# Kernel tuning notes

Measured on AMD Instinct MI355X. Metric: run time of the kernel, lower is better.

Reference implementation:

```python
import jax, jax.numpy as jnp
import numpy as np
from jax import lax

B, N, D = 8, 1024, 768      # batch, tokens, feature dim
H, Y = 12, 64               # heads, head dim
M = 3072                    # hopfield memories (4*D)
STEPS = 12                  # descent steps (module default)
ALPHA = 0.1                 # SGD step size (module default)
BETA = 1.0 / np.sqrt(Y)     # attention inverse temperature
EPS = 1e-5


def setup_inputs() -> dict:
    key = jax.random.key(0)
    k0, k1, k2, k3 = jax.random.split(key, 4)
    return {
        "x": jax.random.normal(k0, (B, N, D), dtype=jnp.float32),
        "ln_gamma": jnp.ones((D,), dtype=jnp.float32),
        "ln_beta": jnp.zeros((D,), dtype=jnp.float32),
        "wq": jax.random.normal(k1, (H, Y, D), dtype=jnp.float32) * 0.02,
        "wk": jax.random.normal(k2, (H, Y, D), dtype=jnp.float32) * 0.02,
        "xi": jax.random.normal(k3, (M, D), dtype=jnp.float32) * 0.02,
    }


def _layer_norm(x, gamma, beta):
    mu = jnp.mean(x, axis=-1, keepdims=True)
    var = jnp.var(x, axis=-1, keepdims=True)
    return gamma * (x - mu) * lax.rsqrt(var + EPS) + beta


def _energy(g, wq, wk, xi):
    # Attention energy: A[b,h,m,n] = sum_y K_{hy m} Q_{hy n}
    q = jnp.einsum("hyd,bnd->bhny", wq, g)
    k = jnp.einsum("hyd,bnd->bhny", wk, g)
    logits = BETA * jnp.einsum("bhmy,bhny->bhmn", k, q)  # [B,H,N(keys),N(queries)]
    e_att = -(1.0 / BETA) * jnp.sum(jax.scipy.special.logsumexp(logits, axis=2))
    # Hopfield energy: -0.5 * sum relu(xi @ g)^2
    hid = jnp.einsum("md,bnd->bnm", xi, g)
    e_hn = -0.5 * jnp.sum(jnp.square(jax.nn.relu(hid)))
    return e_att + e_hn


_energy_grad = jax.grad(_energy)


def reference(x, ln_gamma, ln_beta, wq, wk, xi):
    def step(x, _):
        g = _layer_norm(x, ln_gamma, ln_beta)  # grad taken w.r.t. g, not through LN
        grad = _energy_grad(g, wq, wk, xi)
        return x - ALPHA * grad, None

    x, _ = lax.scan(step, x, None, length=STEPS)
    return x
```

## Files before the change

kernel.cpp:

```cpp
#include <hip/hip_runtime.h>
#include <math.h>

#define B_ 8
#define N_ 1024
#define D_ 768
#define H_ 12
#define Y_ 64
#define M_ 3072
#define STEPS_ 12
#define ALPHA_ 0.1f
#define BETA_ 0.125f
#define EPS_ 1e-5f

typedef __attribute__((ext_vector_type(8))) short bf16x8;
typedef __attribute__((ext_vector_type(8))) unsigned short u16x8;
typedef __attribute__((ext_vector_type(4))) float f32x4;

__device__ inline unsigned short f2bf(float f) {
  union { float f; unsigned int u; } v; v.f = f;
  unsigned int r = (v.u + 0x7fffu + ((v.u >> 16) & 1u)) >> 16;
  return (unsigned short)r;
}

__device__ inline void async_copy16(const void* g, void* l) {
  __builtin_amdgcn_global_load_lds(
      (const __attribute__((address_space(1))) unsigned int*)g,
      (__attribute__((address_space(3))) unsigned int*)l, 16, 0, 0);
}

__device__ inline int xcd_remap(int bid, int nwg) {
  const int qd = nwg >> 3, rm = nwg & 7;
  const int xcd = bid & 7, idx = bid >> 3;
  return (xcd < rm ? xcd * (qd + 1) : rm * (qd + 1) + (xcd - rm) * qd) + idx;
}

__global__ __launch_bounds__(256) void ln_kernel(const float* __restrict__ x,
    const float* __restrict__ gamma, const float* __restrict__ beta,
    unsigned short* __restrict__ g) {
  const int row = blockIdx.x;
  const int t = threadIdx.x;
  const float* xr = x + (size_t)row * D_;
  float v0 = xr[t], v1 = xr[t + 256], v2 = xr[t + 512];
  float s = v0 + v1 + v2;
  float sq = v0 * v0 + v1 * v1 + v2 * v2;
  #pragma unroll
  for (int off = 1; off < 64; off <<= 1) {
    s += __shfl_xor(s, off);
    sq += __shfl_xor(sq, off);
  }
  __shared__ float ss[4], ssq[4];
  const int wid = t >> 6;
  if ((t & 63) == 0) { ss[wid] = s; ssq[wid] = sq; }
  __syncthreads();
  s = ss[0] + ss[1] + ss[2] + ss[3];
  sq = ssq[0] + ssq[1] + ssq[2] + ssq[3];
  const float mu = s * (1.0f / D_);
  const float var = sq * (1.0f / D_) - mu * mu;
  const float r = rsqrtf(var + EPS_);
  unsigned short* gr = g + (size_t)row * D_;
  gr[t]       = f2bf(gamma[t]       * (v0 - mu) * r + beta[t]);
  gr[t + 256] = f2bf(gamma[t + 256] * (v1 - mu) * r + beta[t + 256]);
  gr[t + 512] = f2bf(gamma[t + 512] * (v2 - mu) * r + beta[t + 512]);
}

__global__ __launch_bounds__(256) void cvt_bf16(const float* __restrict__ in,
    unsigned short* __restrict__ out, int n) {
  int i = blockIdx.x * 256 + threadIdx.x;
  if (i < n) out[i] = f2bf(in[i]);
}

__global__ __launch_bounds__(256) void transpose_cvt(const float* __restrict__ in,
    unsigned short* __restrict__ out, int R, int C, int ldo, int koff) {
  __shared__ float tile[32][33];
  const int c0 = blockIdx.x * 32, r0 = blockIdx.y * 32;
  const int tx = threadIdx.x & 31, ty = threadIdx.x >> 5;
  #pragma unroll
  for (int i = 0; i < 32; i += 8)
    tile[ty + i][tx] = in[(size_t)(r0 + ty + i) * C + c0 + tx];
  __syncthreads();
  #pragma unroll
  for (int i = 0; i < 32; i += 8)
    out[(size_t)(c0 + ty + i) * ldo + koff + r0 + tx] = f2bf(tile[tx][ty + i]);
}

__global__ __launch_bounds__(256) void transpose_head(
    const unsigned short* __restrict__ in, int ld, int coff,
    unsigned short* __restrict__ out) {
  __shared__ unsigned short tile[64][68];
  const int n0 = blockIdx.x * 64;
  const int h = blockIdx.y;
  const int b = blockIdx.z;
  const int t = threadIdx.x;
  {
    const int tok = t >> 2, c0 = (t & 3) * 16;
    const unsigned short* src = in + ((size_t)(b * N_ + n0 + tok)) * ld + coff + h * Y_ + c0;
    u16x8 v0 = *(const u16x8*)src;
    u16x8 v1 = *(const u16x8*)(src + 8);
    #pragma unroll
    for (int i = 0; i < 8; ++i) {
      tile[tok][c0 + i] = v0[i];
      tile[tok][c0 + 8 + i] = v1[i];
    }
  }
  __syncthreads();
  {
    const int y = t >> 2, tb = (t & 3) * 16;
    u16x8 o0, o1;
    #pragma unroll
    for (int i = 0; i < 8; ++i) {
      o0[i] = tile[tb + i][y];
      o1[i] = tile[tb + 8 + i][y];
    }
    unsigned short* dst = out + ((size_t)((b * H_ + h) * Y_ + y)) * N_ + n0 + tb;
    *(u16x8*)dst = o0;
    *(u16x8*)(dst + 8) = o1;
  }
}

template <bool RELU>
__global__ __launch_bounds__(256) void gemm128(
    const unsigned short* __restrict__ A, const unsigned short* __restrict__ Bm,
    unsigned short* __restrict__ C, int N, int K, int gridN) {
  __shared__ __align__(16) unsigned short As[128 * 64];
  __shared__ __align__(16) unsigned short Bs[128 * 64];
  const int t = threadIdx.x;
  const int f = xcd_remap(blockIdx.x, gridDim.x);
  const int n0 = (f % gridN) * 128;
  const int m0 = (f / gridN) * 128;
  const int w = t >> 6;
  const int l = t & 63;
  const int wr = (w >> 1) * 64;
  const int wc = (w & 1) * 64;

  f32x4 acc[4][4];
  #pragma unroll
  for (int m = 0; m < 4; ++m)
    #pragma unroll
    for (int n = 0; n < 4; ++n) {
      f32x4 z = {0.f, 0.f, 0.f, 0.f};
      acc[m][n] = z;
    }

  for (int kt = 0; kt < K; kt += 64) {
    #pragma unroll
    for (int i = 0; i < 4; ++i) {
      const int flat = i * 4096 + t * 16;
      const int row = flat >> 7;
      const int slog = ((flat >> 4) & 7) ^ (row & 7);
      async_copy16(A + (size_t)(m0 + row) * K + kt + slog * 8, (char*)As + flat);
      async_copy16(Bm + (size_t)(n0 + row) * K + kt + slog * 8, (char*)Bs + flat);
    }
    __syncthreads();
    #pragma unroll
    for (int kk = 0; kk < 2; ++kk) {
      bf16x8 a[4], b[4];
      const int lr = l & 15;
      const int sl = kk * 4 + (l >> 4);
      #pragma unroll
      for (int m = 0; m < 4; ++m) {
        const int row = wr + m * 16 + lr;
        a[m] = *(const bf16x8*)((const char*)As + row * 128 + ((sl ^ (row & 7)) << 4));
      }
      #pragma unroll
      for (int n = 0; n < 4; ++n) {
        const int row = wc + n * 16 + lr;
        b[n] = *(const bf16x8*)((const char*)Bs + row * 128 + ((sl ^ (row & 7)) << 4));
      }
      #pragma unroll
      for (int m = 0; m < 4; ++m)
        #pragma unroll
        for (int n = 0; n < 4; ++n)
          acc[m][n] = __builtin_amdgcn_mfma_f32_16x16x32_bf16(a[m], b[n], acc[m][n], 0, 0, 0);
    }
    __syncthreads();
  }

  const int cr = (l >> 4) * 4;
  const int cc = l & 15;
  #pragma unroll
  for (int m = 0; m < 4; ++m)
    #pragma unroll
    for (int n = 0; n < 4; ++n) {
      const int col = n0 + wc + n * 16 + cc;
      #pragma unroll
      for (int j = 0; j < 4; ++j) {
        const int row = m0 + wr + m * 16 + cr + j;
        float v = acc[m][n][j];
        if (RELU) v = v > 0.f ? v : 0.f;
        C[(size_t)row * N + col] = f2bf(v);
      }
    }
}

__global__ __launch_bounds__(256) void gemm_update(
    const unsigned short* __restrict__ A1,
    const unsigned short* __restrict__ A2,
    const unsigned short* __restrict__ B2,
    float* __restrict__ x,
    float alpha) {
  __shared__ __align__(16) unsigned short As[128 * 64];
  __shared__ __align__(16) unsigned short Bs[64 * 64];
  const int t = threadIdx.x;
  const int f = xcd_remap(blockIdx.x, gridDim.x);
  const int n0 = (f % 12) * 64;
  const int m0 = (f / 12) * 128;
  const int w = t >> 6;
  const int l = t & 63;
  const int wr = (w >> 1) * 64;
  const int wc = (w & 1) * 32;

  f32x4 acc[4][2];
  #pragma unroll
  for (int m = 0; m < 4; ++m)
    #pragma unroll
    for (int n = 0; n < 2; ++n) {
      f32x4 z = {0.f, 0.f, 0.f, 0.f};
      acc[m][n] = z;
    }

  for (int kt = 0; kt < 4608; kt += 64) {
    #pragma unroll
    for (int i = 0; i < 4; ++i) {
      const int flat = i * 4096 + t * 16;
      const int row = flat >> 7;
      const int slog = ((flat >> 4) & 7) ^ (row & 7);
      const unsigned short* src = (kt < 1536)
          ? A1 + (size_t)(m0 + row) * 1536 + kt + slog * 8
          : A2 + (size_t)(m0 + row) * 3072 + (kt - 1536) + slog * 8;
      async_copy16(src, (char*)As + flat);
    }
    #pragma unroll
    for (int i = 0; i < 2; ++i) {
      const int flat = i * 4096 + t * 16;
      const int row = flat >> 7;
      const int slog = ((flat >> 4) & 7) ^ (row & 7);
      async_copy16(B2 + (size_t)(n0 + row) * 4608 + kt + slog * 8, (char*)Bs + flat);
    }
    __syncthreads();
    #pragma unroll
    for (int kk = 0; kk < 2; ++kk) {
      bf16x8 a[4], b[2];
      const int lr = l & 15;
      const int sl = kk * 4 + (l >> 4);
      #pragma unroll
      for (int m = 0; m < 4; ++m) {
        const int row = wr + m * 16 + lr;
        a[m] = *(const bf16x8*)((const char*)As + row * 128 + ((sl ^ (row & 7)) << 4));
      }
      #pragma unroll
      for (int n = 0; n < 2; ++n) {
        const int row = wc + n * 16 + lr;
        b[n] = *(const bf16x8*)((const char*)Bs + row * 128 + ((sl ^ (row & 7)) << 4));
      }
      #pragma unroll
      for (int m = 0; m < 4; ++m)
        #pragma unroll
        for (int n = 0; n < 2; ++n)
          acc[m][n] = __builtin_amdgcn_mfma_f32_16x16x32_bf16(a[m], b[n], acc[m][n], 0, 0, 0);
    }
    __syncthreads();
  }

  const int cr = (l >> 4) * 4;
  const int cc = l & 15;
  #pragma unroll
  for (int m = 0; m < 4; ++m)
    #pragma unroll
    for (int n = 0; n < 2; ++n) {
      const int col = n0 + wc + n * 16 + cc;
      #pragma unroll
      for (int j = 0; j < 4; ++j) {
        const int row = m0 + wr + m * 16 + cr + j;
        float* cp = x + (size_t)row * 768 + col;
        *cp += alpha * acc[m][n][j];
      }
    }
}

__global__ __launch_bounds__(256) void attn1_mfma(
    const unsigned short* __restrict__ qk, const unsigned short* __restrict__ kT,
    unsigned short* __restrict__ AqAk, float* __restrict__ lse) {
  __shared__ __align__(16) unsigned short Ks[64 * 64];
  __shared__ __align__(16) unsigned short KTs[64 * 64];
  __shared__ __align__(16) unsigned short Ps[4 * 16 * 64];
  const int n0 = blockIdx.x * 64;
  const int h = blockIdx.y;
  const int b = blockIdx.z;
  const int t = threadIdx.x;
  const int w = t >> 6;
  const int l = t & 63;
  const int g = l >> 4;
  const int ql = l & 15;
  char* psw = (char*)(Ps + w * 1024);
  const int LD = 1536;

  bf16x8 qf[2];
  {
    const unsigned short* qrow =
        qk + ((size_t)(b * N_ + n0 + w * 16 + ql)) * LD + h * Y_;
    qf[0] = *(const bf16x8*)(qrow + g * 8);
    qf[1] = *(const bf16x8*)(qrow + 32 + g * 8);
  }
  const unsigned short* kbase = qk + (size_t)b * N_ * LD + 768 + h * Y_;
  const unsigned short* kTbase = kT + ((size_t)(b * H_ + h)) * Y_ * N_;

  f32x4 acc[4];
  #pragma unroll
  for (int yf = 0; yf < 4; ++yf) { f32x4 z = {0.f,0.f,0.f,0.f}; acc[yf] = z; }
  float mmax = -1e30f, lsum = 0.f;

  for (int mc = 0; mc < N_; mc += 64) {
    #pragma unroll
    for (int i = 0; i < 2; ++i) {
      const int flat = i * 4096 + t * 16;
      const int row = flat >> 7;
      const int slog = ((flat >> 4) & 7) ^ (row & 7);
      async_copy16(kbase + (size_t)(mc + row) * LD + slog * 8, (char*)Ks + flat);
    }
    #pragma unroll
    for (int i = 0; i < 2; ++i) {
      const int flat = i * 4096 + t * 16;
      const int row = flat >> 7;
      const int slog = ((flat >> 4) & 7) ^ (row & 7);
      async_copy16(kTbase + (size_t)row * N_ + mc + slog * 8, (char*)KTs + flat);
    }
    __syncthreads();

    f32x4 s[4];
    #pragma unroll
    for (int f = 0; f < 4; ++f) {
      f32x4 z = {0.f,0.f,0.f,0.f}; s[f] = z;
      #pragma unroll
      for (int ks = 0; ks < 2; ++ks) {
        const int key = f * 16 + ql;
        bf16x8 a = *(const bf16x8*)((const char*)Ks + key * 128 +
                                    (((ks * 4 + g) ^ (key & 7)) << 4));
        s[f] = __builtin_amdgcn_mfma_f32_16x16x32_bf16(a, qf[ks], s[f], 0, 0, 0);
      }
    }
    float sv[4][4];
    float rm = -1e30f;
    #pragma unroll
    for (int f = 0; f < 4; ++f)
      #pragma unroll
      for (int j = 0; j < 4; ++j) {
        sv[f][j] = s[f][j] * BETA_;
        rm = fmaxf(rm, sv[f][j]);
      }
    rm = fmaxf(rm, __shfl_xor(rm, 16));
    rm = fmaxf(rm, __shfl_xor(rm, 32));
    const float nm = fmaxf(mmax, rm);
    const float sc = __expf(mmax - nm);
    float rs = 0.f;
    float pv[4][4];
    #pragma unroll
    for (int f = 0; f < 4; ++f)
      #pragma unroll
      for (int j = 0; j < 4; ++j) {
        pv[f][j] = __expf(sv[f][j] - nm);
        rs += pv[f][j];
      }
    rs += __shfl_xor(rs, 16);
    rs += __shfl_xor(rs, 32);
    lsum = lsum * sc + rs;
    mmax = nm;
    #pragma unroll
    for (int yf = 0; yf < 4; ++yf) acc[yf] *= sc;
    #pragma unroll
    for (int f = 0; f < 4; ++f) {
      unsigned long long pk =
          (unsigned long long)f2bf(pv[f][0]) |
          ((unsigned long long)f2bf(pv[f][1]) << 16) |
          ((unsigned long long)f2bf(pv[f][2]) << 32) |
          ((unsigned long long)f2bf(pv[f][3]) << 48);
      const int sl = (f * 4 + g) ^ ((ql & 7) << 1);
      *(unsigned long long*)(psw + ql * 128 + sl * 8) = pk;
    }
    #pragma unroll
    for (int ks2 = 0; ks2 < 2; ++ks2) {
      const int sl2 = (ks2 * 8 + g * 2) ^ ((ql & 7) << 1);
      bf16x8 pa = *(const bf16x8*)(psw + ql * 128 + sl2 * 8);
      #pragma unroll
      for (int yf = 0; yf < 4; ++yf) {
        const int y = yf * 16 + ql;
        bf16x8 bk = *(const bf16x8*)((const char*)KTs + y * 128 +
                                     (((ks2 * 4 + g) ^ (y & 7)) << 4));
        acc[yf] = __builtin_amdgcn_mfma_f32_16x16x32_bf16(pa, bk, acc[yf], 0, 0, 0);
      }
    }
    __syncthreads();
  }

  float linv[4];
  #pragma unroll
  for (int j = 0; j < 4; ++j)
    linv[j] = 1.0f / __shfl(lsum, (g << 4) + g * 4 + j);
  #pragma unroll
  for (int yf = 0; yf < 4; ++yf)
    #pragma unroll
    for (int j = 0; j < 4; ++j) {
      const int row = n0 + w * 16 + g * 4 + j;
      AqAk[((size_t)(b * N_ + row)) * LD + h * Y_ + yf * 16 + ql] =
          f2bf(acc[yf][j] * linv[j]);
    }
  if (g == 0)
    lse[((size_t)b * H_ + h) * N_ + n0 + w * 16 + ql] = mmax + __logf(lsum);
}

__global__ __launch_bounds__(256) void attn2_mfma(
    const unsigned short* __restrict__ qk, const unsigned short* __restrict__ qT,
    const float* __restrict__ lse, unsigned short* __restrict__ AqAk) {
  __shared__ __align__(16) unsigned short Qs[64 * 64];
  __shared__ __align__(16) unsigned short QTs[64 * 64];
  __shared__ __align__(16) unsigned short Ws[4 * 16 * 64];
  __shared__ float lse_s[64];
  const int m0 = blockIdx.x * 64;
  const int h = blockIdx.y;
  const int b = blockIdx.z;
  const int t = threadIdx.x;
  const int w = t >> 6;
  const int l = t & 63;
  const int g = l >> 4;
  const int ql = l & 15;
  char* wsw = (char*)(Ws + w * 1024);
  const int LD = 1536;

  bf16x8 ka[2];
  {
    const unsigned short* krow =
        qk + ((size_t)(b * N_ + m0 + w * 16 + ql)) * LD + 768 + h * Y_;
    ka[0] = *(const bf16x8*)(krow + g * 8);
    ka[1] = *(const bf16x8*)(krow + 32 + g * 8);
  }
  const unsigned short* qbase = qk + (size_t)b * N_ * LD + h * Y_;
  const unsigned short* qTbase = qT + ((size_t)(b * H_ + h)) * Y_ * N_;
  const float* lbase = lse + ((size_t)b * H_ + h) * N_;

  f32x4 acc[4];
  #pragma unroll
  for (int yf = 0; yf < 4; ++yf) { f32x4 z = {0.f,0.f,0.f,0.f}; acc[yf] = z; }

  for (int nc = 0; nc < N_; nc += 64) {
    #pragma unroll
    for (int i = 0; i < 2; ++i) {
      const int flat = i * 4096 + t * 16;
      const int row = flat >> 7;
      const int slog = ((flat >> 4) & 7) ^ (row & 7);
      async_copy16(qbase + (size_t)(nc + row) * LD + slog * 8, (char*)Qs + flat);
    }
    #pragma unroll
    for (int i = 0; i < 2; ++i) {
      const int flat = i * 4096 + t * 16;
      const int row = flat >> 7;
      const int slog = ((flat >> 4) & 7) ^ (row & 7);
      async_copy16(qTbase + (size_t)row * N_ + nc + slog * 8, (char*)QTs + flat);
    }
    if (t < 64) lse_s[t] = lbase[nc + t];
    __syncthreads();

    f32x4 s[4];
    #pragma unroll
    for (int f = 0; f < 4; ++f) {
      f32x4 z = {0.f,0.f,0.f,0.f}; s[f] = z;
      #pragma unroll
      for (int ks = 0; ks < 2; ++ks) {
        const int qr = f * 16 + ql;
        bf16x8 a = *(const bf16x8*)((const char*)Qs + qr * 128 +
                                    (((ks * 4 + g) ^ (qr & 7)) << 4));
        s[f] = __builtin_amdgcn_mfma_f32_16x16x32_bf16(a, ka[ks], s[f], 0, 0, 0);
      }
    }
    #pragma unroll
    for (int f = 0; f < 4; ++f) {
      unsigned short w4[4];
      #pragma unroll
      for (int j = 0; j < 4; ++j) {
        const float wv = __expf(s[f][j] * BETA_ - lse_s[f * 16 + g * 4 + j]);
        w4[j] = f2bf(wv);
      }
      unsigned long long pk =
          (unsigned long long)w4[0] | ((unsigned long long)w4[1] << 16) |
          ((unsigned long long)w4[2] << 32) | ((unsigned long long)w4[3] << 48);
      const int sl = (f * 4 + g) ^ ((ql & 7) << 1);
      *(unsigned long long*)(wsw + ql * 128 + sl * 8) = pk;
    }
    #pragma unroll
    for (int ks2 = 0; ks2 < 2; ++ks2) {
      const int sl2 = (ks2 * 8 + g * 2) ^ ((ql & 7) << 1);
      bf16x8 wa = *(const bf16x8*)(wsw + ql * 128 + sl2 * 8);
      #pragma unroll
      for (int yf = 0; yf < 4; ++yf) {
        const int y = yf * 16 + ql;
        bf16x8 bq = *(const bf16x8*)((const char*)QTs + y * 128 +
                                     (((ks2 * 4 + g) ^ (y & 7)) << 4));
        acc[yf] = __builtin_amdgcn_mfma_f32_16x16x32_bf16(wa, bq, acc[yf], 0, 0, 0);
      }
    }
    __syncthreads();
  }

  #pragma unroll
  for (int yf = 0; yf < 4; ++yf)
    #pragma unroll
    for (int j = 0; j < 4; ++j) {
      const int row = m0 + w * 16 + g * 4 + j;
      AqAk[((size_t)(b * N_ + row)) * LD + 768 + h * Y_ + yf * 16 + ql] =
          f2bf(acc[yf][j]);
    }
}

extern "C" void kernel_launch(void* const* d_in, const int* in_sizes, int n_in,
                              void* d_out, int out_size, void* d_ws, size_t ws_size,
                              hipStream_t stream) {
  const float* x0    = (const float*)d_in[0];
  const float* gamma = (const float*)d_in[1];
  const float* beta  = (const float*)d_in[2];
  const float* wq    = (const float*)d_in[3];
  const float* wk    = (const float*)d_in[4];
  const float* xi    = (const float*)d_in[5];
  float* x = (float*)d_out;

  const size_t SZ = (size_t)B_ * N_ * D_;
  char* wsp = (char*)d_ws;
  size_t off = 0;
  auto alloc = [&](size_t bytes) -> void* {
    off = (off + 255) & ~(size_t)255;
    void* p = wsp + off;
    off += bytes;
    return p;
  };
  unsigned short* g_bf   = (unsigned short*)alloc(SZ * 2);
  unsigned short* qk_bf  = (unsigned short*)alloc(SZ * 2 * 2);
  unsigned short* AqAk   = (unsigned short*)alloc(SZ * 2 * 2);
  unsigned short* qT_bf  = (unsigned short*)alloc(SZ * 2);
  unsigned short* kT_bf  = (unsigned short*)alloc(SZ * 2);
  float*          lse    = (float*)alloc((size_t)B_ * H_ * N_ * 4);
  unsigned short* wqk_bf = (unsigned short*)alloc((size_t)2 * D_ * D_ * 2);
  unsigned short* xi_bf  = (unsigned short*)alloc((size_t)M_ * D_ * 2);
  unsigned short* B2_bf  = (unsigned short*)alloc((size_t)D_ * (2 * D_ + M_) * 2);
  off = (off + 255) & ~(size_t)255;
  unsigned short* hid_bf = (unsigned short*)(wsp + off);
  size_t avail = ws_size > off ? ws_size - off : 0;
  long rmax = (long)(avail / ((size_t)M_ * 2));
  int R = (int)((rmax / 128) * 128);
  if (R > B_ * N_) R = B_ * N_;
  if (R < 128) R = 128;

  const int WQN = D_ * D_;
  const int XIN = M_ * D_;
  cvt_bf16<<<(WQN + 255) / 256, 256, 0, stream>>>(wq, wqk_bf, WQN);
  cvt_bf16<<<(WQN + 255) / 256, 256, 0, stream>>>(wk, wqk_bf + (size_t)D_ * D_, WQN);
  cvt_bf16<<<(XIN + 255) / 256, 256, 0, stream>>>(xi, xi_bf, XIN);
  const int LDB2 = 2 * D_ + M_;
  transpose_cvt<<<dim3(D_ / 32, D_ / 32), 256, 0, stream>>>(wq, B2_bf, D_, D_, LDB2, 0);
  transpose_cvt<<<dim3(D_ / 32, D_ / 32), 256, 0, stream>>>(wk, B2_bf, D_, D_, LDB2, D_);
  transpose_cvt<<<dim3(D_ / 32, M_ / 32), 256, 0, stream>>>(xi, B2_bf, M_, D_, LDB2, 2 * D_);

  hipMemcpyAsync(x, x0, SZ * sizeof(float), hipMemcpyDeviceToDevice, stream);

  const int MN = B_ * N_;
  for (int step = 0; step < STEPS_; ++step) {
    ln_kernel<<<MN, 256, 0, stream>>>(x, gamma, beta, g_bf);
    gemm128<false><<<(1536 / 128) * (MN / 128), 256, 0, stream>>>(
        g_bf, wqk_bf, qk_bf, 1536, D_, 1536 / 128);
    transpose_head<<<dim3(N_ / 64, H_, B_), 256, 0, stream>>>(qk_bf, 1536, 0, qT_bf);
    transpose_head<<<dim3(N_ / 64, H_, B_), 256, 0, stream>>>(qk_bf, 1536, 768, kT_bf);
    attn1_mfma<<<dim3(N_ / 64, H_, B_), 256, 0, stream>>>(qk_bf, kT_bf, AqAk, lse);
    attn2_mfma<<<dim3(N_ / 64, H_, B_), 256, 0, stream>>>(qk_bf, qT_bf, lse, AqAk);
    for (int r0 = 0; r0 < MN; r0 += R) {
      const int rows = (MN - r0) < R ? (MN - r0) : R;
      gemm128<true><<<(M_ / 128) * (rows / 128), 256, 0, stream>>>(
          g_bf + (size_t)r0 * D_, xi_bf, hid_bf, M_, D_, M_ / 128);
      gemm_update<<<(D_ / 64) * (rows / 128), 256, 0, stream>>>(
          AqAk + (size_t)r0 * 1536, hid_bf, B2_bf, x + (size_t)r0 * D_, ALPHA_);
    }
  }
}
```

Baseline: 3.338 ms.

## Fuse Q/K transposes into projection GEMM epilogue and widen attention key tiles

The QK projection GEMM now also writes transposed per-head Q and K layouts straight from its epilogue, which removes the two separate transpose_head launches and their global re-reads. Both attention kernels now process 128 keys/queries per loop iteration instead of 64, which halves the number of barriers and loop trips. This roughly doubles their shared memory use and register pressure. MFMA sections are wrapped in s_setprio to favour matrix issue. Risks include lower occupancy and scattered 8-byte transposed stores from the GEMM epilogue.

```diff
diff --git a/kernel.cpp b/kernel.cpp
--- a/kernel.cpp
+++ b/kernel.cpp
@@ -83,44 +83,11 @@
     out[(size_t)(c0 + ty + i) * ldo + koff + r0 + tx] = f2bf(tile[tx][ty + i]);
 }
 
-__global__ __launch_bounds__(256) void transpose_head(
-    const unsigned short* __restrict__ in, int ld, int coff,
-    unsigned short* __restrict__ out) {
-  __shared__ unsigned short tile[64][68];
-  const int n0 = blockIdx.x * 64;
-  const int h = blockIdx.y;
-  const int b = blockIdx.z;
-  const int t = threadIdx.x;
-  {
-    const int tok = t >> 2, c0 = (t & 3) * 16;
-    const unsigned short* src = in + ((size_t)(b * N_ + n0 + tok)) * ld + coff + h * Y_ + c0;
-    u16x8 v0 = *(const u16x8*)src;
-    u16x8 v1 = *(const u16x8*)(src + 8);
-    #pragma unroll
-    for (int i = 0; i < 8; ++i) {
-      tile[tok][c0 + i] = v0[i];
-      tile[tok][c0 + 8 + i] = v1[i];
-    }
-  }
-  __syncthreads();
-  {
-    const int y = t >> 2, tb = (t & 3) * 16;
-    u16x8 o0, o1;
-    #pragma unroll
-    for (int i = 0; i < 8; ++i) {
-      o0[i] = tile[tb + i][y];
-      o1[i] = tile[tb + 8 + i][y];
-    }
-    unsigned short* dst = out + ((size_t)((b * H_ + h) * Y_ + y)) * N_ + n0 + tb;
-    *(u16x8*)dst = o0;
-    *(u16x8*)(dst + 8) = o1;
-  }
-}
-
-template <bool RELU>
+template <bool RELU, bool WRT>
 __global__ __launch_bounds__(256) void gemm128(
     const unsigned short* __restrict__ A, const unsigned short* __restrict__ Bm,
-    unsigned short* __restrict__ C, int N, int K, int gridN) {
+    unsigned short* __restrict__ C, int N, int K, int gridN,
+    unsigned short* __restrict__ qT, unsigned short* __restrict__ kT) {
   __shared__ __align__(16) unsigned short As[128 * 64];
   __shared__ __align__(16) unsigned short Bs[128 * 64];
   const int t = threadIdx.x;
@@ -182,12 +149,22 @@
     #pragma unroll
     for (int n = 0; n < 4; ++n) {
       const int col = n0 + wc + n * 16 + cc;
+      unsigned long long pk = 0;
       #pragma unroll
       for (int j = 0; j < 4; ++j) {
         const int row = m0 + wr + m * 16 + cr + j;
         float v = acc[m][n][j];
         if (RELU) v = v > 0.f ? v : 0.f;
-        C[(size_t)row * N + col] = f2bf(v);
+        const unsigned short bv = f2bf(v);
+        C[(size_t)row * N + col] = bv;
+        if (WRT) pk |= (unsigned long long)bv << (16 * j);
+      }
+      if (WRT) {
+        const int row0 = m0 + wr + m * 16 + cr;
+        const int bb = row0 >> 10, nn = row0 & 1023;
+        const int hy = (col < 768) ? col : (col - 768);
+        unsigned short* T = (col < 768) ? qT : kT;
+        *(unsigned long long*)(T + ((size_t)bb * 768 + hy) * N_ + nn) = pk;
       }
     }
 }
@@ -280,9 +257,9 @@
 __global__ __launch_bounds__(256) void attn1_mfma(
     const unsigned short* __restrict__ qk, const unsigned short* __restrict__ kT,
     unsigned short* __restrict__ AqAk, float* __restrict__ lse) {
-  __shared__ __align__(16) unsigned short Ks[64 * 64];
-  __shared__ __align__(16) unsigned short KTs[64 * 64];
-  __shared__ __align__(16) unsigned short Ps[4 * 16 * 64];
+  __shared__ __align__(16) unsigned short Ks[128 * 64];
+  __shared__ __align__(16) unsigned short KTs[64 * 128];
+  __shared__ __align__(16) unsigned short Ps[4 * 16 * 128];
   const int n0 = blockIdx.x * 64;
   const int h = blockIdx.y;
   const int b = blockIdx.z;
@@ -291,7 +268,7 @@
   const int l = t & 63;
   const int g = l >> 4;
   const int ql = l & 15;
-  char* psw = (char*)(Ps + w * 1024);
+  char* psw = (char*)(Ps + w * 2048);
   const int LD = 1536;
 
   bf16x8 qf[2];
@@ -309,26 +286,27 @@
   for (int yf = 0; yf < 4; ++yf) { f32x4 z = {0.f,0.f,0.f,0.f}; acc[yf] = z; }
   float mmax = -1e30f, lsum = 0.f;
 
-  for (int mc = 0; mc < N_; mc += 64) {
-    #pragma unroll
-    for (int i = 0; i < 2; ++i) {
+  for (int mc = 0; mc < N_; mc += 128) {
+    #pragma unroll
+    for (int i = 0; i < 4; ++i) {
       const int flat = i * 4096 + t * 16;
       const int row = flat >> 7;
       const int slog = ((flat >> 4) & 7) ^ (row & 7);
       async_copy16(kbase + (size_t)(mc + row) * LD + slog * 8, (char*)Ks + flat);
     }
     #pragma unroll
-    for (int i = 0; i < 2; ++i) {
-      const int flat = i * 4096 + t * 16;
-      const int row = flat >> 7;
-      const int slog = ((flat >> 4) & 7) ^ (row & 7);
+    for (int i = 0; i < 4; ++i) {
+      const int flat = i * 4096 + t * 16;
+      const int row = flat >> 8;
+      const int slog = ((flat >> 4) & 15) ^ (row & 7);
       async_copy16(kTbase + (size_t)row * N_ + mc + slog * 8, (char*)KTs + flat);
     }
     __syncthreads();
 
-    f32x4 s[4];
-    #pragma unroll
-    for (int f = 0; f < 4; ++f) {
+    f32x4 s[8];
+    __builtin_amdgcn_s_setprio(1);
+    #pragma unroll
+    for (int f = 0; f < 8; ++f) {
       f32x4 z = {0.f,0.f,0.f,0.f}; s[f] = z;
       #pragma unroll
       for (int ks = 0; ks < 2; ++ks) {
@@ -338,56 +316,57 @@
         s[f] = __builtin_amdgcn_mfma_f32_16x16x32_bf16(a, qf[ks], s[f], 0, 0, 0);
       }
     }
-    float sv[4][4];
+    __builtin_amdgcn_s_setprio(0);
     float rm = -1e30f;
     #pragma unroll
-    for (int f = 0; f < 4; ++f)
+    for (int f = 0; f < 8; ++f)
       #pragma unroll
       for (int j = 0; j < 4; ++j) {
-        sv[f][j] = s[f][j] * BETA_;
-        rm = fmaxf(rm, sv[f][j]);
+        const float v = s[f][j] * BETA_;
+        s[f][j] = v;
+        rm = fmaxf(rm, v);
       }
     rm = fmaxf(rm, __shfl_xor(rm, 16));
     rm = fmaxf(rm, __shfl_xor(rm, 32));
     const float nm = fmaxf(mmax, rm);
     const float sc = __expf(mmax - nm);
     float rs = 0.f;
-    float pv[4][4];
-    #pragma unroll
-    for (int f = 0; f < 4; ++f)
+    #pragma unroll
+    for (int f = 0; f < 8; ++f) {
+      unsigned short p4[4];
       #pragma unroll
       for (int j = 0; j < 4; ++j) {
-        pv[f][j] = __expf(sv[f][j] - nm);
-        rs += pv[f][j];
-      }
+        const float pvj = __expf(s[f][j] - nm);
+        rs += pvj;
+        p4[j] = f2bf(pvj);
+      }
+      unsigned long long pk = (unsigned long long)p4[0] |
+          ((unsigned long long)p4[1] << 16) |
+          ((unsigned long long)p4[2] << 32) |
+          ((unsigned long long)p4[3] << 48);
+      const int sl = (f * 4 + g) ^ ((ql & 7) << 1);
+      *(unsigned long long*)(psw + ql * 256 + sl * 8) = pk;
+    }
     rs += __shfl_xor(rs, 16);
     rs += __shfl_xor(rs, 32);
     lsum = lsum * sc + rs;
     mmax = nm;
     #pragma unroll
     for (int yf = 0; yf < 4; ++yf) acc[yf] *= sc;
-    #pragma unroll
-    for (int f = 0; f < 4; ++f) {
-      unsigned long long pk =
-          (unsigned long long)f2bf(pv[f][0]) |
-          ((unsigned long long)f2bf(pv[f][1]) << 16) |
-          ((unsigned long long)f2bf(pv[f][2]) << 32) |
-          ((unsigned long long)f2bf(pv[f][3]) << 48);
-      const int sl = (f * 4 + g) ^ ((ql & 7) << 1);
-      *(unsigned long long*)(psw + ql * 128 + sl * 8) = pk;
-    }
-    #pragma unroll
-    for (int ks2 = 0; ks2 < 2; ++ks2) {
+    __builtin_amdgcn_s_setprio(1);
+    #pragma unroll
+    for (int ks2 = 0; ks2 < 4; ++ks2) {
       const int sl2 = (ks2 * 8 + g * 2) ^ ((ql & 7) << 1);
-      bf16x8 pa = *(const bf16x8*)(psw + ql * 128 + sl2 * 8);
+      bf16x8 pa = *(const bf16x8*)(psw + ql * 256 + sl2 * 8);
       #pragma unroll
       for (int yf = 0; yf < 4; ++yf) {
         const int y = yf * 16 + ql;
-        bf16x8 bk = *(const bf16x8*)((const char*)KTs + y * 128 +
+        bf16x8 bk = *(const bf16x8*)((const char*)KTs + y * 256 +
                                      (((ks2 * 4 + g) ^ (y & 7)) << 4));
         acc[yf] = __builtin_amdgcn_mfma_f32_16x16x32_bf16(pa, bk, acc[yf], 0, 0, 0);
       }
     }
+    __builtin_amdgcn_s_setprio(0);
     __syncthreads();
   }
 
@@ -410,10 +389,10 @@
 __global__ __launch_bounds__(256) void attn2_mfma(
     const unsigned short* __restrict__ qk, const unsigned short* __restrict__ qT,
     const float* __restrict__ lse, unsigned short* __restrict__ AqAk) {
-  __shared__ __align__(16) unsigned short Qs[64 * 64];
-  __shared__ __align__(16) unsigned short QTs[64 * 64];
-  __shared__ __align__(16) unsigned short Ws[4 * 16 * 64];
-  __shared__ float lse_s[64];
+  __shared__ __align__(16) unsigned short Qs[128 * 64];
+  __shared__ __align__(16) unsigned short QTs[64 * 128];
+  __shared__ __align__(16) unsigned short Ws[4 * 16 * 128];
+  __shared__ float lse_s[128];
   const int m0 = blockIdx.x * 64;
   const int h = blockIdx.y;
   const int b = blockIdx.z;
@@ -422,7 +401,7 @@
   const int l = t & 63;
   const int g = l >> 4;
   const int ql = l & 15;
-  char* wsw = (char*)(Ws + w * 1024);
+  char* wsw = (char*)(Ws + w * 2048);
   const int LD = 1536;
 
   bf16x8 ka[2];
@@ -440,27 +419,28 @@
   #pragma unroll
   for (int yf = 0; yf < 4; ++yf) { f32x4 z = {0.f,0.f,0.f,0.f}; acc[yf] = z; }
 
-  for (int nc = 0; nc < N_; nc += 64) {
-    #pragma unroll
-    for (int i = 0; i < 2; ++i) {
+  for (int nc = 0; nc < N_; nc += 128) {
+    #pragma unroll
+    for (int i = 0; i < 4; ++i) {
       const int flat = i * 4096 + t * 16;
       const int row = flat >> 7;
       const int slog = ((flat >> 4) & 7) ^ (row & 7);
       async_copy16(qbase + (size_t)(nc + row) * LD + slog * 8, (char*)Qs + flat);
     }
     #pragma unroll
-    for (int i = 0; i < 2; ++i) {
-      const int flat = i * 4096 + t * 16;
-      const int row = flat >> 7;
-      const int slog = ((flat >> 4) & 7) ^ (row & 7);
+    for (int i = 0; i < 4; ++i) {
+      const int flat = i * 4096 + t * 16;
+      const int row = flat >> 8;
+      const int slog = ((flat >> 4) & 15) ^ (row & 7);
       async_copy16(qTbase + (size_t)row * N_ + nc + slog * 8, (char*)QTs + flat);
     }
-    if (t < 64) lse_s[t] = lbase[nc + t];
-    __syncthreads();
-
-    f32x4 s[4];
-    #pragma unroll
-    for (int f = 0; f < 4; ++f) {
+    if (t < 128) lse_s[t] = lbase[nc + t];
+    __syncthreads();
+
+    f32x4 s[8];
+    __builtin_amdgcn_s_setprio(1);
+    #pragma unroll
+    for (int f = 0; f < 8; ++f) {
       f32x4 z = {0.f,0.f,0.f,0.f}; s[f] = z;
       #pragma unroll
       for (int ks = 0; ks < 2; ++ks) {
@@ -470,8 +450,9 @@
         s[f] = __builtin_amdgcn_mfma_f32_16x16x32_bf16(a, ka[ks], s[f], 0, 0, 0);
       }
     }
-    #pragma unroll
-    for (int f = 0; f < 4; ++f) {
+    __builtin_amdgcn_s_setprio(0);
+    #pragma unroll
+    for (int f = 0; f < 8; ++f) {
       unsigned short w4[4];
       #pragma unroll
       for (int j = 0; j < 4; ++j) {
@@ -482,20 +463,22 @@
           (unsigned long long)w4[0] | ((unsigned long long)w4[1] << 16) |
           ((unsigned long long)w4[2] << 32) | ((unsigned long long)w4[3] << 48);
       const int sl = (f * 4 + g) ^ ((ql & 7) << 1);
-      *(unsigned long long*)(wsw + ql * 128 + sl * 8) = pk;
-    }
-    #pragma unroll
-    for (int ks2 = 0; ks2 < 2; ++ks2) {
+      *(unsigned long long*)(wsw + ql * 256 + sl * 8) = pk;
+    }
+    __builtin_amdgcn_s_setprio(1);
+    #pragma unroll
+    for (int ks2 = 0; ks2 < 4; ++ks2) {
       const int sl2 = (ks2 * 8 + g * 2) ^ ((ql & 7) << 1);
-      bf16x8 wa = *(const bf16x8*)(wsw + ql * 128 + sl2 * 8);
+      bf16x8 wa = *(const bf16x8*)(wsw + ql * 256 + sl2 * 8);
       #pragma unroll
       for (int yf = 0; yf < 4; ++yf) {
         const int y = yf * 16 + ql;
-        bf16x8 bq = *(const bf16x8*)((const char*)QTs + y * 128 +
+        bf16x8 bq = *(const bf16x8*)((const char*)QTs + y * 256 +
                                      (((ks2 * 4 + g) ^ (y & 7)) << 4));
         acc[yf] = __builtin_amdgcn_mfma_f32_16x16x32_bf16(wa, bq, acc[yf], 0, 0, 0);
       }
     }
+    __builtin_amdgcn_s_setprio(0);
     __syncthreads();
   }
 
@@ -561,16 +544,14 @@
   const int MN = B_ * N_;
   for (int step = 0; step < STEPS_; ++step) {
     ln_kernel<<<MN, 256, 0, stream>>>(x, gamma, beta, g_bf);
-    gemm128<false><<<(1536 / 128) * (MN / 128), 256, 0, stream>>>(
-        g_bf, wqk_bf, qk_bf, 1536, D_, 1536 / 128);
-    transpose_head<<<dim3(N_ / 64, H_, B_), 256, 0, stream>>>(qk_bf, 1536, 0, qT_bf);
-    transpose_head<<<dim3(N_ / 64, H_, B_), 256, 0, stream>>>(qk_bf, 1536, 768, kT_bf);
+    gemm128<false, true><<<(1536 / 128) * (MN / 128), 256, 0, stream>>>(
+        g_bf, wqk_bf, qk_bf, 1536, D_, 1536 / 128, qT_bf, kT_bf);
     attn1_mfma<<<dim3(N_ / 64, H_, B_), 256, 0, stream>>>(qk_bf, kT_bf, AqAk, lse);
     attn2_mfma<<<dim3(N_ / 64, H_, B_), 256, 0, stream>>>(qk_bf, qT_bf, lse, AqAk);
     for (int r0 = 0; r0 < MN; r0 += R) {
       const int rows = (MN - r0) < R ? (MN - r0) : R;
-      gemm128<true><<<(M_ / 128) * (rows / 128), 256, 0, stream>>>(
-          g_bf + (size_t)r0 * D_, xi_bf, hid_bf, M_, D_, M_ / 128);
+      gemm128<true, false><<<(M_ / 128) * (rows / 128), 256, 0, stream>>>(
+          g_bf + (size_t)r0 * D_, xi_bf, hid_bf, M_, D_, M_ / 128, nullptr, nullptr);
       gemm_update<<<(D_ / 64) * (rows / 128), 256, 0, stream>>>(
           AqAk + (size_t)r0 * 1536, hid_bf, B2_bf, x + (size_t)r0 * D_, ALPHA_);
     }
```

After: 3.282 ms. About the same (-1.7%).
